# Performance work log

Measured on AMD Instinct MI355X. Metric: run time of the kernel, lower is better.

## Reference

```python
import jax, jax.numpy as jnp
import numpy as np

B, L, HID = 2, 2048, 2048
H, D = 16, 128
BASE = 10000.0
EPS = 1e-6
SOFT_CAP = 30.0
NEG = jnp.finfo(jnp.float32).min


def setup_inputs() -> dict:
    key = jax.random.key(0)
    ks = jax.random.split(key, 8)
    s = 0.02
    return {
        "hidden_states": jax.random.normal(ks[0], (B, L, HID), jnp.float32),
        "Wq": jax.random.normal(ks[1], (HID, HID), jnp.float32) * s,
        "Wk": jax.random.normal(ks[2], (HID, HID), jnp.float32) * s,
        "Wv": jax.random.normal(ks[3], (HID, HID), jnp.float32) * s,
        "Wo": jax.random.normal(ks[4], (HID, HID), jnp.float32) * s,
        "q_norm_w": jnp.zeros((HID,), jnp.float32),
        "k_norm_w": jnp.zeros((HID,), jnp.float32),
        "k_bias": jax.random.normal(ks[5], (H, D), jnp.float32) * s,
        "v_bias": jax.random.normal(ks[6], (H, D), jnp.float32) * s,
        "positions": jnp.broadcast_to(jnp.arange(L, dtype=jnp.int32), (B, L)),
        "attention_mask": jnp.ones((B, L, L), dtype=bool),
    }


def _rms_norm(x, w):
    var = jnp.mean(jnp.square(x.astype(jnp.float32)), axis=-1, keepdims=True)
    y = x * jax.lax.rsqrt(var + EPS)
    return ((1.0 + w) * y).astype(x.dtype)


def _rope(x, cos, sin):
    # x: [B, L, H, D]; cos/sin: [B, L, 1, D//2]; neox style
    x1, x2 = jnp.split(x, 2, axis=-1)
    return jnp.concatenate([x1 * cos - x2 * sin, x2 * cos + x1 * sin], axis=-1)


def reference(hidden_states, Wq, Wk, Wv, Wo, q_norm_w, k_norm_w, k_bias, v_bias,
              positions, attention_mask):
    fan_in = HID ** -0.5
    q = (hidden_states @ Wq.T) * fan_in
    k = (hidden_states @ Wk.T) * fan_in
    v = (hidden_states @ Wv.T) * fan_in

    # qk-norm on flat hidden dim (GiddRMSNorm over hidden_size)
    q = _rms_norm(q, q_norm_w)
    k = _rms_norm(k, k_norm_w)

    q = q.reshape(B, L, H, D)
    k = k.reshape(B, L, H, D)
    v = v.reshape(B, L, H, D)

    # rotary embedding (neox, rotary_dim == head_dim)
    inv = 1.0 / (BASE ** (jnp.arange(0, D, 2, dtype=jnp.float32) / D))  # [D//2]
    ang = positions.astype(jnp.float32)[..., None] * inv  # [B, L, D//2]
    cos = jnp.cos(ang)[:, :, None, :]
    sin = jnp.sin(ang)[:, :, None, :]
    q = _rope(q, cos, sin)
    k = _rope(k, cos, sin)

    # learned attention biases on k/v per head
    k = k + k_bias[None, None, :, :]
    v = v + v_bias[None, None, :, :]

    q = q.transpose(0, 2, 1, 3)  # [B, H, L, D]
    k = k.transpose(0, 2, 1, 3)
    v = v.transpose(0, 2, 1, 3)

    scale = D ** -0.5
    scores = jnp.einsum('bhqd,bhkd->bhqk', q * scale, k)
    scores = SOFT_CAP * jnp.tanh(scores / SOFT_CAP)
    scores = jnp.where(attention_mask[:, None, :, :], scores, NEG)
    probs = jax.nn.softmax(scores.astype(jnp.float32), axis=-1).astype(scores.dtype)
    out = jnp.einsum('bhqk,bhkd->bhqd', probs, v)
    out = out.transpose(0, 2, 1, 3).reshape(B, L, HID)
    return (out @ Wo.T) * fan_in
```

## Files before the change

### kernel.cpp

```cpp
#include <hip/hip_runtime.h>
#include <math.h>

#define B_  2
#define L_  2048
#define HID_ 2048
#define H_  16
#define D_  128
#define FAN_IN 0.02209708691207961f
#define SM_SCALE 0.08838834764831845f
#define LOG2E 1.4426950408889634

typedef _Float16 f16;
typedef unsigned int u32;
typedef __attribute__((ext_vector_type(4))) _Float16 f16x4;
typedef __attribute__((ext_vector_type(8))) _Float16 f16x8;
typedef __attribute__((ext_vector_type(4))) float f32x4;

#define CAP_C0 0.12751738960681625f
#define CAP_C1 (-3.690028637e-7f)
#define CAP_C2 (1.28121e-12f)
#define FIXED_M2 8.0f

__device__ __forceinline__ float fexp2(float x) {
#if __has_builtin(__builtin_amdgcn_exp2f)
    return __builtin_amdgcn_exp2f(x);
#else
    return exp2f(x);
#endif
}
__device__ __forceinline__ float frcp(float x) {
#if __has_builtin(__builtin_amdgcn_rcpf)
    return __builtin_amdgcn_rcpf(x);
#else
    return 1.0f / x;
#endif
}
__device__ __forceinline__ void gload_lds16(const void* g, void* l) {
#if __has_builtin(__builtin_amdgcn_global_load_lds)
    __builtin_amdgcn_global_load_lds(
        (const __attribute__((address_space(1))) u32*)g,
        (__attribute__((address_space(3))) u32*)l, 16, 0, 0);
#else
    *(uint4*)l = *(const uint4*)g;
#endif
}

__global__ __launch_bounds__(256) void cvt5(
    const float* __restrict__ s0, const float* __restrict__ s1,
    const float* __restrict__ s2, const float* __restrict__ s3,
    const float* __restrict__ s4,
    f16* __restrict__ d0, f16* __restrict__ d1, f16* __restrict__ d2,
    f16* __restrict__ d3, f16* __restrict__ d4, int n0, int nw)
{
    const int seg = blockIdx.y;
    const float* s = seg==0?s0:seg==1?s1:seg==2?s2:seg==3?s3:s4;
    f16* d = seg==0?d0:seg==1?d1:seg==2?d2:seg==3?d3:d4;
    const int n = (seg==0) ? n0 : nw;
    const int i = (blockIdx.x*256 + threadIdx.x)*8;
    if (i >= n) return;
    float4 a = *(const float4*)&s[i];
    float4 b = *(const float4*)&s[i+4];
    f16x8 o;
    o[0]=(f16)a.x; o[1]=(f16)a.y; o[2]=(f16)a.z; o[3]=(f16)a.w;
    o[4]=(f16)b.x; o[5]=(f16)b.y; o[6]=(f16)b.z; o[7]=(f16)b.w;
    *(f16x8*)&d[i] = o;
}

__global__ __launch_bounds__(512, 2) void gemm8p_qkv(
    const f16* __restrict__ A,
    const f16* __restrict__ Bq, const f16* __restrict__ Bk,
    const f16* __restrict__ Bv,
    f16* __restrict__ C0, f16* __restrict__ C1,
    f16* __restrict__ Vt, const float* __restrict__ vb,
    int M, int N, int K, float scale)
{
    __shared__ f16 lds[65536];
    const f16* Bw = blockIdx.z==0 ? Bq : blockIdx.z==1 ? Bk : Bv;

    const int t = threadIdx.x;
    const int w = t >> 6, l = t & 63;
    const int lane15 = l & 15, quad = l >> 4;
    const int m0 = blockIdx.y * 256, n0 = blockIdx.x * 256;
    const int wmr = (w >> 2) * 128;
    const int wnc = (w & 3) * 64;
    const int xslot = (quad ^ ((lane15 >> 1) & 3)) * 8;

    const int srow = t >> 2;
    const int sc   = t & 3;
    const int cs0 = (sc ^ ((srow >> 1) & 3)) * 8;
    const int cs1 = (sc ^ (((128 + srow) >> 1) & 3)) * 8;
    const f16* Ag0 = A  + (size_t)(m0 + srow) * K + cs0;
    const f16* Ag1 = A  + (size_t)(m0 + 128 + srow) * K + cs1;
    const f16* Bg0 = Bw + (size_t)(n0 + srow) * K + cs0;
    const f16* Bg1 = Bw + (size_t)(n0 + 128 + srow) * K + cs1;
    f16* const ldst = lds + t * 8;

#define STAGE_A(KOFF, S, NB) {                                           \
    gload_lds16(Ag0 + (KOFF) + (S)*32, ldst + (NB) + (S)*16384);         \
    gload_lds16(Ag1 + (KOFF) + (S)*32, ldst + (NB) + (S)*16384 + 4096); }
#define STAGE_B(KOFF, S, NB) {                                           \
    gload_lds16(Bg0 + (KOFF) + (S)*32, ldst + (NB) + (S)*16384 + 8192);  \
    gload_lds16(Bg1 + (KOFF) + (S)*32, ldst + (NB) + (S)*16384 + 12288); }

    f32x4 acc[8][4] = {};
    f16x8 bfr[4];

#define PHASE(H, S, ...)                                                  \
    {                                                                     \
        const f16* Ab_ = lds + bufo + (S)*16384;                          \
        f16x8 af[4];                                                      \
        _Pragma("unroll")                                                 \
        for (int i = 0; i < 4; i++) {                                     \
            const int r = wmr + (H)*64 + i*16 + lane15;                   \
            af[i] = *(const f16x8*)&Ab_[r*32 + xslot];                    \
        }                                                                 \
        if ((H) == 0) {                                                   \
            const f16* Bb_ = Ab_ + 8192;                                  \
            _Pragma("unroll")                                             \
            for (int j = 0; j < 4; j++) {                                 \
                const int r = wnc + j*16 + lane15;                        \
                bfr[j] = *(const f16x8*)&Bb_[r*32 + xslot];               \
            }                                                             \
        }                                                                 \
        __VA_ARGS__;                                                      \
        __builtin_amdgcn_s_barrier();                                     \
        __builtin_amdgcn_s_setprio(1);                                    \
        _Pragma("unroll")                                                 \
        for (int i = 0; i < 4; i++)                                       \
            _Pragma("unroll")                                             \
            for (int j = 0; j < 4; j++)                                   \
                acc[(H)*4+i][j] = __builtin_amdgcn_mfma_f32_16x16x32_f16( \
                    af[i], bfr[j], acc[(H)*4+i][j], 0, 0, 0);             \
        __builtin_amdgcn_s_setprio(0);                                    \
    }

    STAGE_A(0, 0, 0); STAGE_B(0, 0, 0);
    STAGE_A(0, 1, 0); STAGE_B(0, 1, 0);
    asm volatile("s_waitcnt vmcnt(4)" ::: "memory");
    __builtin_amdgcn_s_barrier();

    const int NT = K >> 6;
    for (int kt = 0; kt < NT; kt++) {
        const int bufo = (kt & 1) * 32768;
        const int nb   = ((kt + 1) & 1) * 32768;
        const int kn   = (kt + 1) * 64;
        const bool pf  = (kt + 1 < NT);

        PHASE(0, 0, if (pf) STAGE_A(kn, 0, nb))
        __builtin_amdgcn_s_barrier();
        PHASE(1, 0, if (pf) STAGE_B(kn, 0, nb))
        asm volatile("s_waitcnt vmcnt(4)" ::: "memory");
        __builtin_amdgcn_s_barrier();
        PHASE(0, 1, if (pf) STAGE_A(kn, 1, nb))
        __builtin_amdgcn_s_barrier();
        PHASE(1, 1, if (pf) STAGE_B(kn, 1, nb))
        asm volatile("s_waitcnt vmcnt(4)" ::: "memory");
        __builtin_amdgcn_s_barrier();
    }

#undef PHASE
#undef STAGE_A
#undef STAGE_B

    if (blockIdx.z == 2) {
#pragma unroll
        for (int fi = 0; fi < 8; fi++)
#pragma unroll
            for (int j = 0; j < 4; j++) {
                const int col = n0 + wnc + j*16 + lane15;
                const int row0 = m0 + wmr + fi*16 + quad*4;
                const int b = row0 >> 11, ll = row0 & 2047;
                const int bh = (b << 4) + (col >> 7);
                const float bias = vb[col];
                f16x4 ph;
#pragma unroll
                for (int r = 0; r < 4; r++)
                    ph[r] = (f16)(acc[fi][j][r] * scale + bias);
                *(f16x4*)&Vt[((size_t)(bh*128 + (col & 127)))*(size_t)L_ + ll] = ph;
            }
    } else {
        f16* Cout = blockIdx.z==0 ? C0 : C1;
#pragma unroll
        for (int fi = 0; fi < 8; fi++)
#pragma unroll
            for (int j = 0; j < 4; j++) {
                const int col = n0 + wnc + j*16 + lane15;
#pragma unroll
                for (int r = 0; r < 4; r++) {
                    const int row = m0 + wmr + fi*16 + quad*4 + r;
                    Cout[(size_t)row*N + col] = (f16)(acc[fi][j][r] * scale);
                }
            }
    }
}

__global__ __launch_bounds__(256) void gemm16_f32out(
    const f16* __restrict__ A, const f16* __restrict__ Bw,
    float* __restrict__ Cout, int M, int N, int K, float scale)
{
    __shared__ f16 As[128*32];
    __shared__ f16 Bs[128*32];
    const int t = threadIdx.x;
    const int w = t >> 6, l = t & 63;
    const int lane15 = l & 15, quad = l >> 4;
    const int m0 = blockIdx.y*128, n0 = blockIdx.x*128;
    const int wm = (w & 1)*64, wn = (w >> 1)*64;

    const int srow = t >> 2;
    const int scol = (((t & 3) ^ ((t >> 3) & 3))) * 8;
    const f16* Ag = A  + (size_t)(m0 + srow)*K + scol;
    const f16* Bg = Bw + (size_t)(n0 + srow)*K + scol;
    f16* Al = As + t*8;
    f16* Bl = Bs + t*8;

    f32x4 acc[4][4] = {};
    for (int k0 = 0; k0 < K; k0 += 32) {
        gload_lds16(Ag + k0,                 Al);
        gload_lds16(Ag + (size_t)64*K + k0,  Al + 2048);
        gload_lds16(Bg + k0,                 Bl);
        gload_lds16(Bg + (size_t)64*K + k0,  Bl + 2048);
        __syncthreads();
        f16x8 af[4], bf[4];
#pragma unroll
        for (int i = 0; i < 4; i++) {
            const int ra = wm + i*16 + lane15;
            const int rb = wn + i*16 + lane15;
            af[i] = *(const f16x8*)&As[ra*32 + ((quad ^ ((ra >> 1) & 3)) * 8)];
            bf[i] = *(const f16x8*)&Bs[rb*32 + ((quad ^ ((rb >> 1) & 3)) * 8)];
        }
#pragma unroll
        for (int i = 0; i < 4; i++)
#pragma unroll
            for (int j = 0; j < 4; j++)
                acc[i][j] = __builtin_amdgcn_mfma_f32_16x16x32_f16(af[i], bf[j], acc[i][j], 0, 0, 0);
        __syncthreads();
    }
#pragma unroll
    for (int i = 0; i < 4; i++)
#pragma unroll
        for (int j = 0; j < 4; j++) {
            const int col = n0 + wn + j*16 + lane15;
#pragma unroll
            for (int r = 0; r < 4; r++) {
                const int row = m0 + wm + i*16 + quad*4 + r;
                Cout[(size_t)row*N + col] = acc[i][j][r] * scale;
            }
        }
}

__global__ void rope_table(const int* __restrict__ pos,
                           float* __restrict__ ct, float* __restrict__ st_)
{
    const int r = blockIdx.x, i = threadIdx.x;
    double inv = exp2(-(double)i * (13.287712379549449 / 64.0));
    double a = (double)pos[r] * inv;
    double sd, cd;
    sincos(a, &sd, &cd);
    ct[r*64+i] = (float)cd;
    st_[r*64+i] = (float)sd;
}

__global__ __launch_bounds__(256) void mask_pack(const int* __restrict__ m,
                                                 u32* __restrict__ bits)
{
    const int g = blockIdx.x*256 + threadIdx.x;
    const int* p = m + (size_t)g*32;
    u32 w = 0;
#pragma unroll
    for (int j = 0; j < 8; j++) {
        int4 v = *(const int4*)&p[j*4];
        w |= (v.x!=0 ? 1u:0u) << (j*4+0);
        w |= (v.y!=0 ? 1u:0u) << (j*4+1);
        w |= (v.z!=0 ? 1u:0u) << (j*4+2);
        w |= (v.w!=0 ? 1u:0u) << (j*4+3);
    }
    bits[g] = w;
}

__global__ __launch_bounds__(256) void norm_rope(
    f16* __restrict__ Q, f16* __restrict__ K,
    const float* __restrict__ qw, const float* __restrict__ kw,
    const float* __restrict__ kb,
    const float* __restrict__ ct, const float* __restrict__ st_)
{
    const int r = blockIdx.x;
    const int t = threadIdx.x;
    const size_t base = (size_t)r * HID_;

    const int p0 = t * 4;
    const int hh = p0 >> 6;
    const int i0 = p0 & 63;
    const int c1 = hh * 128 + i0;
    f16x4 q1h = *(f16x4*)&Q[base + c1];
    f16x4 q2h = *(f16x4*)&Q[base + c1 + 64];
    f16x4 k1h = *(f16x4*)&K[base + c1];
    f16x4 k2h = *(f16x4*)&K[base + c1 + 64];
    float q1[4], q2[4], k1[4], k2[4];
#pragma unroll
    for (int j = 0; j < 4; j++) {
        q1[j]=(float)q1h[j]; q2[j]=(float)q2h[j];
        k1[j]=(float)k1h[j]; k2[j]=(float)k2h[j];
    }

    float ssq = 0.f, ssk = 0.f;
#pragma unroll
    for (int j = 0; j < 4; j++) {
        ssq += q1[j]*q1[j] + q2[j]*q2[j];
        ssk += k1[j]*k1[j] + k2[j]*k2[j];
    }
#pragma unroll
    for (int off = 1; off < 64; off <<= 1) {
        ssq += __shfl_xor(ssq, off);
        ssk += __shfl_xor(ssk, off);
    }
    __shared__ float rq[4], rk[4];
    const int wave = t >> 6, lane = t & 63;
    if (lane == 0) { rq[wave] = ssq; rk[wave] = ssk; }
    __syncthreads();
    ssq = rq[0] + rq[1] + rq[2] + rq[3];
    ssk = rk[0] + rk[1] + rk[2] + rk[3];
    const float rsq = rsqrtf(ssq * (1.f / HID_) + 1e-6f);
    const float rsk = rsqrtf(ssk * (1.f / HID_) + 1e-6f);

    float4 cos4 = *(const float4*)&ct[r*64 + i0];
    float4 sin4 = *(const float4*)&st_[r*64 + i0];
    float cc[4] = {cos4.x, cos4.y, cos4.z, cos4.w};
    float ss[4] = {sin4.x, sin4.y, sin4.z, sin4.w};

    f16x4 oq1, oq2, ok1, ok2;
#pragma unroll
    for (int j = 0; j < 4; j++) {
        const float c = cc[j], s = ss[j];
        const float wq1 = 1.f + qw[c1 + j], wq2 = 1.f + qw[c1 + 64 + j];
        const float wk1 = 1.f + kw[c1 + j], wk2 = 1.f + kw[c1 + 64 + j];
        float qa = q1[j] * rsq * wq1, qb = q2[j] * rsq * wq2;
        oq1[j] = (f16)(qa * c - qb * s);
        oq2[j] = (f16)(qb * c + qa * s);
        float ka = k1[j] * rsk * wk1, kbv = k2[j] * rsk * wk2;
        ok1[j] = (f16)(ka * c - kbv * s + kb[c1 + j]);
        ok2[j] = (f16)(kbv * c + ka * s + kb[c1 + 64 + j]);
    }
    *(f16x4*)&Q[base + c1]      = oq1;
    *(f16x4*)&Q[base + c1 + 64] = oq2;
    *(f16x4*)&K[base + c1]      = ok1;
    *(f16x4*)&K[base + c1 + 64] = ok2;
}

__global__ __launch_bounds__(256, 2) void flash16(
    const f16* __restrict__ Qh, const f16* __restrict__ Kh,
    const f16* __restrict__ Vtg, const u32* __restrict__ bits,
    f16* __restrict__ AOh)
{
    __shared__ f16 lds[40960];

    const int t = threadIdx.x;
    const int w = t >> 6, l = t & 63;
    const int lane15 = l & 15, quad = l >> 4;
    const int bh = blockIdx.y;
    const int b = bh >> 4, h = bh & 15;
    const int q0 = blockIdx.x * 128;

    const size_t qkbase = ((size_t)(b*L_))*HID_ + h*128;
    const size_t vbase  = ((size_t)(bh*128))*L_;

#pragma unroll
    for (int i = 0; i < 8; i++) {
        int f = t + i*256;
        int row = f >> 4, c4 = f & 15;
        int c = c4 ^ (row & 15);
        *(uint4*)&lds[row*128 + c4*8] =
            *(const uint4*)&Qh[qkbase + (size_t)(q0 + row)*HID_ + c*8];
    }
    __syncthreads();
    f16x8 qf[2][4];
#pragma unroll
    for (int qt = 0; qt < 2; qt++)
#pragma unroll
        for (int dc = 0; dc < 4; dc++)
            qf[qt][dc] = *(const f16x8*)&lds[(w*32 + qt*16 + lane15)*128
                                             + (((dc*4 + quad) ^ lane15) * 8)];
    __syncthreads();

    {
        f16* Kb = lds;            f16* Vb = lds + 16384;
#pragma unroll
        for (int it = 0; it < 4; it++) {
            int j = w*256 + it*64 + l;
            int krow = j >> 4, kc = (j & 15) ^ (krow & 15);
            gload_lds16(Kh + qkbase + (size_t)krow*HID_ + kc*8, Kb + j*8);
            int vrow = j >> 3, vc = (j & 7) ^ (vrow & 7);
            gload_lds16(Vtg + vbase + (size_t)vrow*L_ + vc*8, Vb + j*8);
        }
    }

    f32x4 oacc[2][8] = {};
    float lsum[2] = {0.f, 0.f};

    for (int kt = 0; kt < 32; kt++) {
        const int k0 = kt * 64;
        __syncthreads();

        if (kt + 1 < 32) {
            const int kn = k0 + 64;
            f16* Kb = lds + ((kt+1) & 1)*8192;
            f16* Vb = lds + 16384 + ((kt+1) & 1)*8192;
#pragma unroll
            for (int it = 0; it < 4; it++) {
                int j = w*256 + it*64 + l;
                int krow = j >> 4, kc = (j & 15) ^ (krow & 15);
                gload_lds16(Kh + qkbase + (size_t)(kn + krow)*HID_ + kc*8, Kb + j*8);
                int vrow = j >> 3, vc = (j & 7) ^ (vrow & 7);
                gload_lds16(Vtg + vbase + (size_t)vrow*L_ + kn + vc*8, Vb + j*8);
            }
        }
        const f16* Kb = lds + (kt & 1)*8192;
        const f16* Vb = lds + 16384 + (kt & 1)*8192;
        f16* Ps = lds + 32768;

        u32 mw[2][2];
#pragma unroll
        for (int qt = 0; qt < 2; qt++) {
            int qrow = q0 + w*32 + qt*16 + lane15;
            const u32* bp = bits + (((size_t)(b*L_ + qrow)) << 6) + (k0 >> 5);
            mw[qt][0] = bp[0];
            mw[qt][1] = bp[1];
        }

        f32x4 st[2][4];
#pragma unroll
        for (int kt2 = 0; kt2 < 4; kt2++) {
            f16x8 kf[4];
#pragma unroll
            for (int dc = 0; dc < 4; dc++)
                kf[dc] = *(const f16x8*)&Kb[(kt2*16 + lane15)*128
                                            + (((dc*4 + quad) ^ lane15) * 8)];
#pragma unroll
            for (int qt = 0; qt < 2; qt++) {
                f32x4 a = {0.f, 0.f, 0.f, 0.f};
#pragma unroll
                for (int dc = 0; dc < 4; dc++)
                    a = __builtin_amdgcn_mfma_f32_16x16x32_f16(kf[dc], qf[qt][dc], a, 0, 0, 0);
                st[qt][kt2] = a;
            }
        }

#pragma unroll
        for (int qt = 0; qt < 2; qt++) {
            const int prow = (w*32 + qt*16 + lane15) * 64;
            float ls = 0.f;
#pragma unroll
            for (int kt2 = 0; kt2 < 4; kt2++) {
                const u32 w_ = mw[qt][kt2 >> 1];
                f16x4 ph;
#pragma unroll
                for (int r = 0; r < 4; r++) {
                    float x = st[qt][kt2][r];
                    float y = x * x;
                    float p5 = fmaf(CAP_C2, y, CAP_C1);
                    float wv = fmaf(p5, y, CAP_C0);
                    float e = fmaf(x, wv, -FIXED_M2);
                    int kk = kt2*16 + quad*4 + r;
                    e = ((w_ >> (kk & 31)) & 1u) ? e : -150.f;
                    float pv = fexp2(e);
                    ls += pv;
                    ph[r] = (f16)pv;
                }
                const int c16s = (kt2*2 + (quad >> 1)) ^ (lane15 & 7);
                *(f16x4*)&Ps[prow + c16s*8 + (quad & 1)*4] = ph;
            }
            lsum[qt] += ls;
        }

        f16x8 pf[2][2];
#pragma unroll
        for (int qt = 0; qt < 2; qt++)
#pragma unroll
            for (int c = 0; c < 2; c++)
                pf[qt][c] = *(const f16x8*)&Ps[(w*32 + qt*16 + lane15)*64
                                               + (((c*4 + quad) ^ (lane15 & 7)) * 8)];
#pragma unroll
        for (int dt = 0; dt < 8; dt++) {
            f16x8 vf[2];
#pragma unroll
            for (int c = 0; c < 2; c++)
                vf[c] = *(const f16x8*)&Vb[(dt*16 + lane15)*64
                                           + (((c*4 + quad) ^ (lane15 & 7)) * 8)];
#pragma unroll
            for (int qt = 0; qt < 2; qt++)
#pragma unroll
                for (int c = 0; c < 2; c++)
                    oacc[qt][dt] = __builtin_amdgcn_mfma_f32_16x16x32_f16(pf[qt][c], vf[c], oacc[qt][dt], 0, 0, 0);
        }
    }

#pragma unroll
    for (int qt = 0; qt < 2; qt++) {
        lsum[qt] += __shfl_xor(lsum[qt], 16);
        lsum[qt] += __shfl_xor(lsum[qt], 32);
    }
    __syncthreads();
    f16* Ot = lds;
#pragma unroll
    for (int qt = 0; qt < 2; qt++) {
#pragma unroll
        for (int r = 0; r < 4; r++) {
            float inv = frcp(__shfl(lsum[qt], quad*4 + r));
            const int row = w*32 + qt*16 + quad*4 + r;
#pragma unroll
            for (int dt = 0; dt < 8; dt++)
                Ot[row*136 + dt*16 + lane15] = (f16)(oacc[qt][dt][r] * inv);
        }
    }
    __syncthreads();
#pragma unroll
    for (int i = 0; i < 8; i++) {
        int f = t + i*256;
        int row = f >> 4, ch = f & 15;
        *(uint4*)&AOh[qkbase + (size_t)(q0 + row)*HID_ + ch*8] =
            *(const uint4*)&Ot[row*136 + ch*8];
    }
}

extern "C" void kernel_launch(void* const* d_in, const int* in_sizes, int n_in,
                              void* d_out, int out_size, void* d_ws, size_t ws_size,
                              hipStream_t stream)
{
    const float* hs  = (const float*)d_in[0];
    const float* Wq  = (const float*)d_in[1];
    const float* Wk  = (const float*)d_in[2];
    const float* Wv  = (const float*)d_in[3];
    const float* Wo  = (const float*)d_in[4];
    const float* qw  = (const float*)d_in[5];
    const float* kw  = (const float*)d_in[6];
    const float* kb  = (const float*)d_in[7];
    const float* vb  = (const float*)d_in[8];
    const int*   pos = (const int*)d_in[9];
    const int*   mask = (const int*)d_in[10];
    float* out = (float*)d_out;

    char* W = (char*)d_ws;
    f16* hs16 = (f16*)(W);
    f16* w16o = (f16*)(W + 16777216);
    f16* w16q = (f16*)(W + 25165824);
    f16* w16k = (f16*)(W + 33554432);
    f16* w16v = (f16*)(W + 41943040);
    f16* Q16  = (f16*)(W + 50331648);
    f16* K16  = (f16*)(W + 67108864);
    f16* Vtg  = (f16*)(W + 83886080);
    float* ct  = (float*)(W + 41943040);
    float* st_ = (float*)(W + 41943040 + 1048576);
    u32*  bits = (u32*) (W + 41943040 + 2097152);
    f16* AOh = hs16;

    const int M = B_ * L_;
    const int nHS = M * HID_;
    const int nW  = HID_ * HID_;

    cvt5<<<dim3(4096, 5), 256, 0, stream>>>(hs, Wq, Wk, Wv, Wo,
                                            hs16, w16q, w16k, w16v, w16o, nHS, nW);

    gemm8p_qkv<<<dim3(HID_/256, M/256, 3), 512, 0, stream>>>(
        hs16, w16q, w16k, w16v, Q16, K16, Vtg, vb, M, HID_, HID_, FAN_IN);

    rope_table<<<M, 64, 0, stream>>>(pos, ct, st_);
    mask_pack<<<1024, 256, 0, stream>>>(mask, bits);

    norm_rope<<<M, 256, 0, stream>>>(Q16, K16, qw, kw, kb, ct, st_);

    flash16<<<dim3(16, 32), 256, 0, stream>>>(Q16, K16, Vtg, bits, AOh);

    gemm16_f32out<<<dim3(HID_/128, M/128), 256, 0, stream>>>(
        AOh, w16o, out, M, HID_, HID_, FAN_IN);
}
```

Measured before the change: 454.9 us.

## Deepen QKV GEMM prefetch pipeline and add XCD-aware block swizzle

Restructures the QKV projection GEMM main loop so that global-to-LDS loads are issued further ahead, with more loads in flight and finer-grained half-stage refills into the double buffer, followed by an explicit drain epilogue. It also remaps the linear block id so blocks that share A/B tiles are placed on the same XCD, which is meant to improve L2 reuse. The aim is to hide memory latency more fully. The cost is more complex waitcnt accounting and hardcoded grid dimensions (8x16x3) in the swizzle.

```diff
diff --git a/kernel.cpp b/kernel.cpp
--- a/kernel.cpp
+++ b/kernel.cpp
@@ -75,12 +75,17 @@
     int M, int N, int K, float scale)
 {
     __shared__ f16 lds[65536];
-    const f16* Bw = blockIdx.z==0 ? Bq : blockIdx.z==1 ? Bk : Bv;
+
+    const u32 lid = blockIdx.x + (blockIdx.y << 3) + (blockIdx.z << 7);
+    const u32 swz = (lid & 7) * 48 + (lid >> 3);
+    const int n0 = (swz & 7) * 256;
+    const int m0 = ((swz >> 3) & 15) * 256;
+    const int z  = swz >> 7;
+    const f16* Bw = z==0 ? Bq : z==1 ? Bk : Bv;
 
     const int t = threadIdx.x;
     const int w = t >> 6, l = t & 63;
     const int lane15 = l & 15, quad = l >> 4;
-    const int m0 = blockIdx.y * 256, n0 = blockIdx.x * 256;
     const int wmr = (w >> 2) * 128;
     const int wnc = (w & 3) * 64;
     const int xslot = (quad ^ ((lane15 >> 1) & 3)) * 8;
@@ -88,26 +93,27 @@
     const int srow = t >> 2;
     const int sc   = t & 3;
     const int cs0 = (sc ^ ((srow >> 1) & 3)) * 8;
-    const int cs1 = (sc ^ (((128 + srow) >> 1) & 3)) * 8;
     const f16* Ag0 = A  + (size_t)(m0 + srow) * K + cs0;
-    const f16* Ag1 = A  + (size_t)(m0 + 128 + srow) * K + cs1;
+    const f16* Ag1 = A  + (size_t)(m0 + 128 + srow) * K + cs0;
     const f16* Bg0 = Bw + (size_t)(n0 + srow) * K + cs0;
-    const f16* Bg1 = Bw + (size_t)(n0 + 128 + srow) * K + cs1;
+    const f16* Bg1 = Bw + (size_t)(n0 + 128 + srow) * K + cs0;
     f16* const ldst = lds + t * 8;
 
-#define STAGE_A(KOFF, S, NB) {                                           \
-    gload_lds16(Ag0 + (KOFF) + (S)*32, ldst + (NB) + (S)*16384);         \
-    gload_lds16(Ag1 + (KOFF) + (S)*32, ldst + (NB) + (S)*16384 + 4096); }
-#define STAGE_B(KOFF, S, NB) {                                           \
-    gload_lds16(Bg0 + (KOFF) + (S)*32, ldst + (NB) + (S)*16384 + 8192);  \
-    gload_lds16(Bg1 + (KOFF) + (S)*32, ldst + (NB) + (S)*16384 + 12288); }
+#define STG_A(BUF, S, KOFF) {                                             \
+    gload_lds16(Ag0 + (KOFF), ldst + (BUF) + (S)*16384);                  \
+    gload_lds16(Ag1 + (KOFF), ldst + (BUF) + (S)*16384 + 4096); }
+#define STG_B(BUF, S, KOFF) {                                             \
+    gload_lds16(Bg0 + (KOFF), ldst + (BUF) + (S)*16384 + 8192);           \
+    gload_lds16(Bg1 + (KOFF), ldst + (BUF) + (S)*16384 + 12288); }
+#define WV(N) asm volatile("s_waitcnt vmcnt(" #N ")" ::: "memory")
+#define BAR() __builtin_amdgcn_s_barrier()
 
     f32x4 acc[8][4] = {};
     f16x8 bfr[4];
 
-#define PHASE(H, S, ...)                                                  \
+#define PHASE(BUFO, S, H, ...)                                            \
     {                                                                     \
-        const f16* Ab_ = lds + bufo + (S)*16384;                          \
+        const f16* Ab_ = lds + (BUFO) + (S)*16384;                        \
         f16x8 af[4];                                                      \
         _Pragma("unroll")                                                 \
         for (int i = 0; i < 4; i++) {                                     \
@@ -134,35 +140,61 @@
         __builtin_amdgcn_s_setprio(0);                                    \
     }
 
-    STAGE_A(0, 0, 0); STAGE_B(0, 0, 0);
-    STAGE_A(0, 1, 0); STAGE_B(0, 1, 0);
-    asm volatile("s_waitcnt vmcnt(4)" ::: "memory");
-    __builtin_amdgcn_s_barrier();
-
-    const int NT = K >> 6;
-    for (int kt = 0; kt < NT; kt++) {
-        const int bufo = (kt & 1) * 32768;
-        const int nb   = ((kt + 1) & 1) * 32768;
-        const int kn   = (kt + 1) * 64;
-        const bool pf  = (kt + 1 < NT);
-
-        PHASE(0, 0, if (pf) STAGE_A(kn, 0, nb))
-        __builtin_amdgcn_s_barrier();
-        PHASE(1, 0, if (pf) STAGE_B(kn, 0, nb))
-        asm volatile("s_waitcnt vmcnt(4)" ::: "memory");
-        __builtin_amdgcn_s_barrier();
-        PHASE(0, 1, if (pf) STAGE_A(kn, 1, nb))
-        __builtin_amdgcn_s_barrier();
-        PHASE(1, 1, if (pf) STAGE_B(kn, 1, nb))
-        asm volatile("s_waitcnt vmcnt(4)" ::: "memory");
-        __builtin_amdgcn_s_barrier();
+    STG_B(0, 0, 0);  STG_A(0, 0, 0);  STG_B(0, 1, 32);  STG_A(0, 1, 32);
+    STG_B(32768, 0, 64);  STG_A(32768, 0, 64);  STG_B(32768, 1, 96);
+    WV(10); BAR();
+
+    const int NIT = (K >> 7) - 1;
+    for (int it = 0; it < NIT; ++it) {
+        const int kB = it * 128;
+        const int k1A = kB + 96;
+        const int kE  = kB + 128;
+        const int kO  = kB + 192;
+
+        PHASE(0,     0, 0, STG_A(32768, 1, k1A))
+        BAR();
+        PHASE(0,     0, 1, STG_B(0,     0, kE))
+        WV(10); BAR();
+        PHASE(0,     1, 0, STG_A(0,     0, kE))
+        BAR();
+        PHASE(0,     1, 1, STG_B(0,     1, kE + 32))
+        WV(10); BAR();
+        PHASE(32768, 0, 0, STG_A(0,     1, kE + 32))
+        BAR();
+        PHASE(32768, 0, 1, STG_B(32768, 0, kO))
+        WV(10); BAR();
+        PHASE(32768, 1, 0, STG_A(32768, 0, kO))
+        BAR();
+        PHASE(32768, 1, 1, STG_B(32768, 1, kO + 32))
+        WV(10); BAR();
+    }
+
+    {
+        const int k1A = NIT * 128 + 96;
+        PHASE(0,     0, 0, STG_A(32768, 1, k1A))
+        BAR();
+        PHASE(0,     0, 1, )
+        WV(8); BAR();
+        PHASE(0,     1, 0, )
+        BAR();
+        PHASE(0,     1, 1, )
+        WV(4); BAR();
+        PHASE(32768, 0, 0, )
+        BAR();
+        PHASE(32768, 0, 1, )
+        WV(0); BAR();
+        PHASE(32768, 1, 0, )
+        BAR();
+        PHASE(32768, 1, 1, )
     }
 
 #undef PHASE
-#undef STAGE_A
-#undef STAGE_B
-
-    if (blockIdx.z == 2) {
+#undef STG_A
+#undef STG_B
+#undef WV
+#undef BAR
+
+    if (z == 2) {
 #pragma unroll
         for (int fi = 0; fi < 8; fi++)
 #pragma unroll
@@ -179,7 +211,7 @@
                 *(f16x4*)&Vt[((size_t)(bh*128 + (col & 127)))*(size_t)L_ + ll] = ph;
             }
     } else {
-        f16* Cout = blockIdx.z==0 ? C0 : C1;
+        f16* Cout = z==0 ? C0 : C1;
 #pragma unroll
         for (int fi = 0; fi < 8; fi++)
 #pragma unroll
```

Result: no change. 456.0 us (+0.2%).
